# Kernel optimization log

Hardware: AMD Instinct MI355X
Metric: run time of the kernel (lower is better)

## Reference

```python
import jax, jax.numpy as jnp
import numpy as np

L, H, N = 4096, 256, 64  # seq_len, hidden_size, hippo_n
EPS = 1e-5


def setup_inputs() -> dict:
    key = jax.random.key(0)
    ks = jax.random.split(key, 8)
    x = jax.random.normal(ks[0], (L, H), jnp.float32)
    # S4D-Lin style initialization for the diagonal SSM (H independent SSMs of state size N)
    Lambda_re = -0.5 * jnp.ones((H, N), jnp.float32)
    Lambda_im = jnp.tile(jnp.pi * jnp.arange(N, dtype=jnp.float32), (H, 1))
    B_re = jnp.ones((H, N), jnp.float32)
    B_im = jnp.zeros((H, N), jnp.float32)
    C_re = jax.random.normal(ks[1], (H, N), jnp.float32) * (0.5 ** 0.5)
    C_im = jax.random.normal(ks[2], (H, N), jnp.float32) * (0.5 ** 0.5)
    D = jax.random.normal(ks[3], (H,), jnp.float32)
    log_step = jax.random.uniform(ks[4], (H,), jnp.float32,
                                  minval=jnp.log(0.001), maxval=jnp.log(0.1))
    ln_w = jnp.ones((H,), jnp.float32)
    ln_b = jnp.zeros((H,), jnp.float32)
    sc = 1.0 / jnp.sqrt(jnp.float32(H))
    W1 = jax.random.normal(ks[5], (H, H), jnp.float32) * sc
    b1 = jnp.zeros((H,), jnp.float32)
    W2 = jax.random.normal(ks[6], (H, H), jnp.float32) * sc
    b2 = jnp.zeros((H,), jnp.float32)
    return {"x": x, "Lambda_re": Lambda_re, "Lambda_im": Lambda_im,
            "B_re": B_re, "B_im": B_im, "C_re": C_re, "C_im": C_im,
            "D": D, "log_step": log_step, "ln_w": ln_w, "ln_b": ln_b,
            "W1": W1, "b1": b1, "W2": W2, "b2": b2}


def reference(x, Lambda_re, Lambda_im, B_re, B_im, C_re, C_im, D, log_step,
              ln_w, ln_b, W1, b1, W2, b2):
    skip = x
    # per-token LayerNorm over the H feature axis (eqx.nn.LayerNorm, eps=1e-5)
    mu = jnp.mean(x, axis=-1, keepdims=True)
    var = jnp.mean(jnp.square(x - mu), axis=-1, keepdims=True)
    xn = (x - mu) / jnp.sqrt(var + EPS) * ln_w + ln_b  # [L, H]

    # ZOH discretization of the diagonal SSM (the cell.ssm(L) step)
    Lam = Lambda_re + 1j * Lambda_im                     # [H, N] complex64
    dt = jnp.exp(log_step)[:, None]                      # [H, 1]
    Ab = jnp.exp(Lam * dt)                               # [H, N]
    Bb = (Ab - 1.0) / Lam * (B_re + 1j * B_im)           # [H, N]
    C = C_re + 1j * C_im                                 # [H, N]

    def step(s, u):  # s: [H, N] complex state, u: [H] input at one time step
        s = Ab * s + Bb * u[:, None]
        y = 2.0 * jnp.einsum('hn,hn->h', C, s).real + D * u
        return s, y

    s0 = jnp.zeros((H, N), jnp.complex64)
    hidden, ys = jax.lax.scan(step, s0, xn)              # ys: [L, H]

    g = jax.nn.gelu(ys)
    out = (g @ W1.T + b1) * jax.nn.sigmoid(g @ W2.T + b2)  # GLU epilogue
    return (hidden, skip + out)
```

## Files before the change

kernel.cpp:

```cpp
#include <hip/hip_runtime.h>
#include <hip/hip_bf16.h>

#define LSEQ 4096
#define HDIM 256
#define NS   64
#define PC   32
#define MC   128

typedef __attribute__((ext_vector_type(8))) short short8;
typedef __attribute__((ext_vector_type(4))) float floatx4;

__device__ __forceinline__ short b16(float x) {
    __hip_bfloat16 h = __float2bfloat16(x);
    return *(reinterpret_cast<short*>(&h));
}
__device__ __forceinline__ unsigned int pk2(float a, float b) {
    return (unsigned int)(unsigned short)b16(a) | ((unsigned int)(unsigned short)b16(b) << 16);
}
__device__ __forceinline__ void cmul(float& xr, float& xi, float yr, float yi) {
    float r = xr * yr - xi * yi;
    float i = xr * yi + xi * yr;
    xr = r; xi = i;
}

__global__ __launch_bounds__(256) void k_pre(const float* __restrict__ x,
                                             const float* __restrict__ lnw,
                                             const float* __restrict__ lnb,
                                             const float* __restrict__ W1,
                                             const float* __restrict__ W2,
                                             float* __restrict__ xnT,
                                             unsigned short* __restrict__ w1b,
                                             unsigned short* __restrict__ w2b) {
    int t = threadIdx.x;
    if (blockIdx.x >= 256) {
        int g = (blockIdx.x - 256) * 256 + t;
        float4 a = ((const float4*)W1)[g];
        float4 c = ((const float4*)W2)[g];
        ushort4 o1, o2;
        o1.x = (unsigned short)b16(a.x); o1.y = (unsigned short)b16(a.y);
        o1.z = (unsigned short)b16(a.z); o1.w = (unsigned short)b16(a.w);
        o2.x = (unsigned short)b16(c.x); o2.y = (unsigned short)b16(c.y);
        o2.z = (unsigned short)b16(c.z); o2.w = (unsigned short)b16(c.w);
        ((ushort4*)w1b)[g] = o1;
        ((ushort4*)w2b)[g] = o2;
        return;
    }
    __shared__ float tile[16][257];
    __shared__ float smu[16], srs[16];
    int l0 = blockIdx.x * 16;
#pragma unroll
    for (int i = 0; i < 16; ++i)
        tile[i][t] = x[(size_t)(l0 + i) * HDIM + t];
    __syncthreads();
    int wv = t >> 6, lane = t & 63;
#pragma unroll
    for (int k = 0; k < 4; ++k) {
        int i = wv * 4 + k;
        float s = 0.f, s2 = 0.f;
#pragma unroll
        for (int q = 0; q < 4; ++q) {
            float v = tile[i][lane + 64 * q];
            s += v; s2 += v * v;
        }
#pragma unroll
        for (int o = 32; o; o >>= 1) {
            s  += __shfl_xor(s, o);
            s2 += __shfl_xor(s2, o);
        }
        if (lane == 0) {
            float m = s * (1.0f / HDIM);
            smu[i] = m;
            srs[i] = rsqrtf(s2 * (1.0f / HDIM) - m * m + 1e-5f);
        }
    }
    __syncthreads();
    float wh = lnw[t], bh = lnb[t];
    float o[16];
#pragma unroll
    for (int i = 0; i < 16; ++i)
        o[i] = (tile[i][t] - smu[i]) * srs[i] * wh + bh;
    float4* dst = (float4*)(xnT + (size_t)t * LSEQ + l0);
#pragma unroll
    for (int k = 0; k < 4; ++k)
        dst[k] = make_float4(o[4 * k], o[4 * k + 1], o[4 * k + 2], o[4 * k + 3]);
}

__device__ __forceinline__ void ssm_consts(const float* Lre, const float* Lim,
                                           const float* Bre, const float* Bim,
                                           float dt, int idx,
                                           float& are, float& aim, float& bre, float& bim) {
    float lre = Lre[idx], lim = Lim[idx];
    float er = expf(lre * dt);
    float sa, ca;
    sincosf(lim * dt, &sa, &ca);
    are = er * ca; aim = er * sa;
    float inv = 1.0f / (lre * lre + lim * lim);
    float nre = are - 1.0f, nim = aim;
    float tre = (nre * lre + nim * lim) * inv;
    float tim = (nim * lre - nre * lim) * inv;
    float br = Bre[idx], bi = Bim[idx];
    bre = tre * br - tim * bi;
    bim = tre * bi + tim * br;
}

__global__ __launch_bounds__(1024) void k_scan(const float* __restrict__ xnT,
                                               const float* __restrict__ Lre,
                                               const float* __restrict__ Lim,
                                               const float* __restrict__ Bre,
                                               const float* __restrict__ Bim,
                                               const float* __restrict__ Cre,
                                               const float* __restrict__ Cim,
                                               const float* __restrict__ Dv,
                                               const float* __restrict__ lstep,
                                               __hip_bfloat16* __restrict__ gb,
                                               float* __restrict__ hid,
                                               int interleaved) {
    __shared__ __align__(16) unsigned char ldsb[60672];
    short* ubf = (short*)(ldsb);
    short* Xm  = (short*)(ldsb + 8704);
    float* Ff  = (float*)(ldsb + 43520);
    short* S0s = (short*)(ldsb + 43520);
    float* Kt  = (float*)(ldsb + 60160);

    int h = blockIdx.x;
    int tid = threadIdx.x;
    int wv = __builtin_amdgcn_readfirstlane(tid) >> 6;
    int lane = tid & 63;
    int l15 = lane & 15, q = lane >> 4;
    int mt = wv >> 1, nt = wv & 1;
    const float* uh = xnT + (size_t)h * LSEQ;

    float dt = expf(lstep[h]);
    float Dh = Dv[h];

    float are, aim, bre, bim;
    ssm_consts(Lre, Lim, Bre, Bim, dt, h * NS + lane, are, aim, bre, bim);
    float cre = Cre[h * NS + lane], cim = Cim[h * NS + lane];

    float A2r = are, A2i = aim;   cmul(A2r, A2i, are, aim);
    float A4r = A2r, A4i = A2i;   cmul(A4r, A4i, A2r, A2i);
    float A8r = A4r, A8i = A4i;   cmul(A8r, A8i, A4r, A4i);
    float A16r = A8r, A16i = A8i;  cmul(A16r, A16i, A8r, A8i);
    float A32r = A16r, A32i = A16i; cmul(A32r, A32i, A16r, A16i);
    float A64r = A32r, A64i = A32i; cmul(A64r, A64i, A32r, A32i);

    {
        int i4 = tid * 4;
        float4 v = *(const float4*)(uh + i4);
        int c = i4 >> 7, col = i4 & 127;
        unsigned int* d = (unsigned int*)(ubf + c * 136 + col);
        d[0] = pk2(v.x, v.y);
        d[1] = pk2(v.z, v.w);
    }

    {
        float cbre = cre * bre - cim * bim;
        float cbim = cre * bim + cim * bre;
        float pr = 1.f, pi = 0.f;
        if (wv & 1) cmul(pr, pi, A8r, A8i);
        if (wv & 2) cmul(pr, pi, A16r, A16i);
        if (wv & 4) cmul(pr, pi, A32r, A32i);
        if (wv & 8) cmul(pr, pi, A64r, A64i);
#pragma unroll
        for (int i = 0; i < 8; ++i) {
            float kj = 2.f * (cbre * pr - cbim * pi);
#pragma unroll
            for (int o = 1; o <= 32; o <<= 1) kj += __shfl_xor(kj, o);
            if (lane == 0) Kt[8 * wv + i] = kj;
            cmul(pr, pi, are, aim);
        }
    }

    {
        int v = 15 - wv;
        float pr = 1.f, pi = 0.f;
        if (v & 1) cmul(pr, pi, A8r, A8i);
        if (v & 2) cmul(pr, pi, A16r, A16i);
        if (v & 4) cmul(pr, pi, A32r, A32i);
        if (v & 8) cmul(pr, pi, A64r, A64i);
        short8 rr, ri;
#pragma unroll
        for (int i = 0; i < 8; ++i) {
            rr[7 - i] = b16(bre * pr - bim * pi);
            ri[7 - i] = b16(bre * pi + bim * pr);
            cmul(pr, pi, are, aim);
        }
        *(short8*)(Xm + lane * 136 + 8 * wv) = rr;
        *(short8*)(Xm + (64 + lane) * 136 + 8 * wv) = ri;
    }
    __syncthreads();

    {
        floatx4 fa = (floatx4){0.f, 0.f, 0.f, 0.f};
#pragma unroll
        for (int ks = 0; ks < 4; ++ks) {
            short8 am = *(short8*)(Xm + (16 * mt + l15) * 136 + 32 * ks + 8 * q);
            short8 bu = *(short8*)(ubf + (16 * nt + l15) * 136 + 32 * ks + 8 * q);
            fa = __builtin_amdgcn_mfma_f32_16x16x32_bf16(am, bu, fa, 0, 0, 0);
        }
        int c = 16 * nt + l15;
        float* fp = Ff + c * 130;
        int sbase = 16 * mt + 4 * q;
#pragma unroll
        for (int reg = 0; reg < 4; ++reg) {
            int s = sbase + reg;
            fp[(mt < 4) ? s : (1 + s)] = fa[reg];
        }
    }
    __syncthreads();

    if (wv == 0) {
        float a128r = A64r, a128i = A64i;
        cmul(a128r, a128i, A64r, A64i);
        float sre = 0.f, sim = 0.f;
        for (int c = 0; c < PC; ++c) {
            float fre = Ff[c * 130 + lane];
            float fim = Ff[c * 130 + 65 + lane];
            ((unsigned int*)(ldsb + 43520 + 272 * c))[lane] = pk2(sre, sim);
            float nr = fmaf(a128r, sre, fmaf(-a128i, sim, fre));
            float ni = fmaf(a128r, sim, fmaf( a128i, sre, fim));
            sre = nr; sim = ni;
        }
        if (interleaved) {
            ((float2*)hid)[h * NS + lane] = make_float2(sre, sim);
        } else {
            hid[h * NS + lane] = sre;
        }
    } else {
        float A15r = A8r, A15i = A8i;
        cmul(A15r, A15i, A4r, A4i);
        cmul(A15r, A15i, A2r, A2i);
        cmul(A15r, A15i, are, aim);
        float pr = 1.f, pi = 0.f;
        if (wv & 1) cmul(pr, pi, are, aim);
        if (wv & 2) cmul(pr, pi, A2r, A2i);
        if (wv & 4) cmul(pr, pi, A4r, A4i);
        if (wv & 8) cmul(pr, pi, A8r, A8i);
#pragma unroll
        for (int i = 0; i < 9; ++i) {
            int t = (wv - 1) + 15 * i;
            if (t < 128) {
                float er =  2.f * (cre * pr - cim * pi);
                float en = -2.f * (cre * pi + cim * pr);
                ((unsigned int*)(ldsb + 8704 + 272 * t))[lane] = pk2(er, en);
            }
            cmul(pr, pi, A15r, A15i);
        }
    }

    floatx4 Y = (floatx4){0.f, 0.f, 0.f, 0.f};
    {
        int row = 16 * mt + l15;
#pragma unroll
        for (int ks = 0; ks < 4; ++ks) {
            short8 ta;
#pragma unroll
            for (int e = 0; e < 8; ++e) {
                int col = 32 * ks + 8 * q + e;
                float kv = Kt[(row - col) & 127];
                ta[e] = (col <= row) ? b16(kv) : (short)0;
            }
            short8 bu = *(short8*)(ubf + (16 * nt + l15) * 136 + 32 * ks + 8 * q);
            Y = __builtin_amdgcn_mfma_f32_16x16x32_bf16(ta, bu, Y, 0, 0, 0);
        }
    }
    __syncthreads();

#pragma unroll
    for (int ks = 0; ks < 4; ++ks) {
        short8 ea = *(short8*)(Xm + (16 * mt + l15) * 136 + 32 * ks + 8 * q);
        short8 sf = *(short8*)(S0s + (16 * nt + l15) * 136 + 32 * ks + 8 * q);
        Y = __builtin_amdgcn_mfma_f32_16x16x32_bf16(ea, sf, Y, 0, 0, 0);
    }

    {
        int c = 16 * nt + l15;
#pragma unroll
        for (int reg = 0; reg < 4; ++reg) {
            int t = 16 * mt + 4 * q + reg;
            int l = c * MC + t;
            float u = uh[l];
            float y = Y[reg] + Dh * u;
            float z = 0.7978845608028654f * fmaf(0.044715f, y * y * y, y);
            float e = __expf(2.f * z);
            float th = 1.f - 2.f / (e + 1.f);
            float gg = 0.5f * y * (1.f + th);
            gb[((size_t)l << 8) + h] = __float2bfloat16(gg);
        }
    }
}

__global__ __launch_bounds__(64) void k_glu_mfma(const unsigned short* __restrict__ gbs,
                                                 const unsigned short* __restrict__ w1b,
                                                 const unsigned short* __restrict__ w2b,
                                                 const float* __restrict__ b1v,
                                                 const float* __restrict__ b2v,
                                                 const float* __restrict__ x,
                                                 float* __restrict__ out) {
    int bx = blockIdx.x;
    int m0 = (bx >> 4) * 32;
    int n0 = (bx & 15) * 16;
    int lane = threadIdx.x;
    int t = lane & 15, q = lane >> 4;

    floatx4 acc[2][2];
    acc[0][0] = (floatx4){0,0,0,0}; acc[0][1] = (floatx4){0,0,0,0};
    acc[1][0] = (floatx4){0,0,0,0}; acc[1][1] = (floatx4){0,0,0,0};

    const unsigned short* A0 = gbs + (size_t)(m0 + t) * HDIM + q * 8;
    const unsigned short* A1 = A0 + 16 * HDIM;
    const unsigned short* B1 = w1b + (size_t)(n0 + t) * HDIM + q * 8;
    const unsigned short* B2 = w2b + (size_t)(n0 + t) * HDIM + q * 8;

#pragma unroll
    for (int ks = 0; ks < 8; ++ks) {
        int off = ks * 32;
        short8 a0 = *(const short8*)(A0 + off);
        short8 a1 = *(const short8*)(A1 + off);
        short8 b1 = *(const short8*)(B1 + off);
        short8 b2 = *(const short8*)(B2 + off);
        acc[0][0] = __builtin_amdgcn_mfma_f32_16x16x32_bf16(a0, b1, acc[0][0], 0, 0, 0);
        acc[1][0] = __builtin_amdgcn_mfma_f32_16x16x32_bf16(a1, b1, acc[1][0], 0, 0, 0);
        acc[0][1] = __builtin_amdgcn_mfma_f32_16x16x32_bf16(a0, b2, acc[0][1], 0, 0, 0);
        acc[1][1] = __builtin_amdgcn_mfma_f32_16x16x32_bf16(a1, b2, acc[1][1], 0, 0, 0);
    }

    int hh = n0 + t;
    float bb1 = b1v[hh], bb2 = b2v[hh];
#pragma unroll
    for (int mt = 0; mt < 2; ++mt) {
#pragma unroll
        for (int reg = 0; reg < 4; ++reg) {
            int l = m0 + mt * 16 + q * 4 + reg;
            float a  = acc[mt][0][reg] + bb1;
            float sg = 1.f / (1.f + __expf(-(acc[mt][1][reg] + bb2)));
            out[(size_t)l * HDIM + hh] = fmaf(a, sg, x[(size_t)l * HDIM + hh]);
        }
    }
}

extern "C" void kernel_launch(void* const* d_in, const int* in_sizes, int n_in,
                              void* d_out, int out_size, void* d_ws, size_t ws_size,
                              hipStream_t stream) {
    (void)in_sizes; (void)n_in; (void)ws_size;
    const float* x     = (const float*)d_in[0];
    const float* Lre   = (const float*)d_in[1];
    const float* Lim   = (const float*)d_in[2];
    const float* Bre   = (const float*)d_in[3];
    const float* Bim   = (const float*)d_in[4];
    const float* Cre   = (const float*)d_in[5];
    const float* Cim   = (const float*)d_in[6];
    const float* Dv    = (const float*)d_in[7];
    const float* lstep = (const float*)d_in[8];
    const float* lnw   = (const float*)d_in[9];
    const float* lnb   = (const float*)d_in[10];
    const float* W1    = (const float*)d_in[11];
    const float* b1    = (const float*)d_in[12];
    const float* W2    = (const float*)d_in[13];
    const float* b2    = (const float*)d_in[14];

    float* ws   = (float*)d_ws;
    float* xnT  = ws;
    unsigned short* gb  = (unsigned short*)(xnT + (size_t)HDIM * LSEQ);
    unsigned short* w1b = gb + (size_t)LSEQ * HDIM;
    unsigned short* w2b = w1b + HDIM * HDIM;

    int interleaved = (out_size == LSEQ * HDIM + 2 * HDIM * NS) ? 1 : 0;
    float* hid  = (float*)d_out;
    float* outp = (float*)d_out + (interleaved ? 2 * HDIM * NS : HDIM * NS);

    k_pre      <<<256 + 64, 256, 0, stream>>>(x, lnw, lnb, W1, W2, xnT, w1b, w2b);
    k_scan     <<<HDIM, 1024, 0, stream>>>(xnT, Lre, Lim, Bre, Bim, Cre, Cim,
                                           Dv, lstep, (__hip_bfloat16*)gb, hid, interleaved);
    k_glu_mfma <<<128 * 16, 64, 0, stream>>>(gb, w1b, w2b, b1, b2, x, outp);
}
```

Baseline: 115.9 us.

## Split SSM scan block per channel into two 512-thread halves

The chunked-scan kernel now launches two 512-thread blocks per hidden channel instead of one 1024-thread block. Each block redundantly builds the chunk-state tables and runs the serial 32-chunk state recurrence, then computes the output for only half of the chunk columns. The D*u skip term is also read from the bf16 LDS copy instead of reloading fp32 from global memory. The aim is better occupancy and spreading the work over more CUs, at the cost of duplicated setup and recurrence work plus slightly lower precision on the skip term.

```diff
diff --git a/kernel.cpp b/kernel.cpp
--- a/kernel.cpp
+++ b/kernel.cpp
@@ -13,6 +13,10 @@
 __device__ __forceinline__ short b16(float x) {
     __hip_bfloat16 h = __float2bfloat16(x);
     return *(reinterpret_cast<short*>(&h));
+}
+__device__ __forceinline__ float bf2f(unsigned short u) {
+    unsigned int v = ((unsigned int)u) << 16;
+    return __uint_as_float(v);
 }
 __device__ __forceinline__ unsigned int pk2(float a, float b) {
     return (unsigned int)(unsigned short)b16(a) | ((unsigned int)(unsigned short)b16(b) << 16);
@@ -103,18 +107,18 @@
     bim = tre * bi + tim * br;
 }
 
-__global__ __launch_bounds__(1024) void k_scan(const float* __restrict__ xnT,
-                                               const float* __restrict__ Lre,
-                                               const float* __restrict__ Lim,
-                                               const float* __restrict__ Bre,
-                                               const float* __restrict__ Bim,
-                                               const float* __restrict__ Cre,
-                                               const float* __restrict__ Cim,
-                                               const float* __restrict__ Dv,
-                                               const float* __restrict__ lstep,
-                                               __hip_bfloat16* __restrict__ gb,
-                                               float* __restrict__ hid,
-                                               int interleaved) {
+__global__ __launch_bounds__(512) void k_scan(const float* __restrict__ xnT,
+                                              const float* __restrict__ Lre,
+                                              const float* __restrict__ Lim,
+                                              const float* __restrict__ Bre,
+                                              const float* __restrict__ Bim,
+                                              const float* __restrict__ Cre,
+                                              const float* __restrict__ Cim,
+                                              const float* __restrict__ Dv,
+                                              const float* __restrict__ lstep,
+                                              __hip_bfloat16* __restrict__ gb,
+                                              float* __restrict__ hid,
+                                              int interleaved) {
     __shared__ __align__(16) unsigned char ldsb[60672];
     short* ubf = (short*)(ldsb);
     short* Xm  = (short*)(ldsb + 8704);
@@ -122,12 +126,11 @@
     short* S0s = (short*)(ldsb + 43520);
     float* Kt  = (float*)(ldsb + 60160);
 
-    int h = blockIdx.x;
+    int h = blockIdx.x >> 1, half = blockIdx.x & 1;
     int tid = threadIdx.x;
     int wv = __builtin_amdgcn_readfirstlane(tid) >> 6;
     int lane = tid & 63;
     int l15 = lane & 15, q = lane >> 4;
-    int mt = wv >> 1, nt = wv & 1;
     const float* uh = xnT + (size_t)h * LSEQ;
 
     float dt = expf(lstep[h]);
@@ -145,66 +148,82 @@
     float A64r = A32r, A64i = A32i; cmul(A64r, A64i, A32r, A32i);
 
     {
-        int i4 = tid * 4;
-        float4 v = *(const float4*)(uh + i4);
-        int c = i4 >> 7, col = i4 & 127;
+        int i8 = tid * 8;
+        float4 v0 = *(const float4*)(uh + i8);
+        float4 v1 = *(const float4*)(uh + i8 + 4);
+        int c = i8 >> 7, col = i8 & 127;
         unsigned int* d = (unsigned int*)(ubf + c * 136 + col);
-        d[0] = pk2(v.x, v.y);
-        d[1] = pk2(v.z, v.w);
+        d[0] = pk2(v0.x, v0.y);
+        d[1] = pk2(v0.z, v0.w);
+        d[2] = pk2(v1.x, v1.y);
+        d[3] = pk2(v1.z, v1.w);
     }
 
     {
         float cbre = cre * bre - cim * bim;
         float cbim = cre * bim + cim * bre;
         float pr = 1.f, pi = 0.f;
-        if (wv & 1) cmul(pr, pi, A8r, A8i);
-        if (wv & 2) cmul(pr, pi, A16r, A16i);
-        if (wv & 4) cmul(pr, pi, A32r, A32i);
-        if (wv & 8) cmul(pr, pi, A64r, A64i);
-#pragma unroll
-        for (int i = 0; i < 8; ++i) {
+        if (wv & 1) cmul(pr, pi, A16r, A16i);
+        if (wv & 2) cmul(pr, pi, A32r, A32i);
+        if (wv & 4) cmul(pr, pi, A64r, A64i);
+#pragma unroll
+        for (int i = 0; i < 16; ++i) {
             float kj = 2.f * (cbre * pr - cbim * pi);
 #pragma unroll
             for (int o = 1; o <= 32; o <<= 1) kj += __shfl_xor(kj, o);
-            if (lane == 0) Kt[8 * wv + i] = kj;
+            if (lane == 0) Kt[16 * wv + i] = kj;
             cmul(pr, pi, are, aim);
         }
     }
 
     {
-        int v = 15 - wv;
+        int v = 7 - wv;
         float pr = 1.f, pi = 0.f;
-        if (v & 1) cmul(pr, pi, A8r, A8i);
-        if (v & 2) cmul(pr, pi, A16r, A16i);
-        if (v & 4) cmul(pr, pi, A32r, A32i);
-        if (v & 8) cmul(pr, pi, A64r, A64i);
-        short8 rr, ri;
-#pragma unroll
-        for (int i = 0; i < 8; ++i) {
-            rr[7 - i] = b16(bre * pr - bim * pi);
-            ri[7 - i] = b16(bre * pi + bim * pr);
+        if (v & 1) cmul(pr, pi, A16r, A16i);
+        if (v & 2) cmul(pr, pi, A32r, A32i);
+        if (v & 4) cmul(pr, pi, A64r, A64i);
+        short8 rrB, riB, rrA, riA;
+#pragma unroll
+        for (int e = 7; e >= 0; --e) {
+            rrB[e] = b16(bre * pr - bim * pi);
+            riB[e] = b16(bre * pi + bim * pr);
             cmul(pr, pi, are, aim);
         }
-        *(short8*)(Xm + lane * 136 + 8 * wv) = rr;
-        *(short8*)(Xm + (64 + lane) * 136 + 8 * wv) = ri;
-    }
-    __syncthreads();
-
-    {
-        floatx4 fa = (floatx4){0.f, 0.f, 0.f, 0.f};
+#pragma unroll
+        for (int e = 7; e >= 0; --e) {
+            rrA[e] = b16(bre * pr - bim * pi);
+            riA[e] = b16(bre * pi + bim * pr);
+            if (e) cmul(pr, pi, are, aim);
+        }
+        *(short8*)(Xm + lane * 136 + 16 * wv) = rrA;
+        *(short8*)(Xm + lane * 136 + 16 * wv + 8) = rrB;
+        *(short8*)(Xm + (64 + lane) * 136 + 16 * wv) = riA;
+        *(short8*)(Xm + (64 + lane) * 136 + 16 * wv + 8) = riB;
+    }
+    __syncthreads();
+
+    {
+        floatx4 fa[2];
+        fa[0] = (floatx4){0.f, 0.f, 0.f, 0.f};
+        fa[1] = (floatx4){0.f, 0.f, 0.f, 0.f};
 #pragma unroll
         for (int ks = 0; ks < 4; ++ks) {
-            short8 am = *(short8*)(Xm + (16 * mt + l15) * 136 + 32 * ks + 8 * q);
-            short8 bu = *(short8*)(ubf + (16 * nt + l15) * 136 + 32 * ks + 8 * q);
-            fa = __builtin_amdgcn_mfma_f32_16x16x32_bf16(am, bu, fa, 0, 0, 0);
-        }
-        int c = 16 * nt + l15;
-        float* fp = Ff + c * 130;
-        int sbase = 16 * mt + 4 * q;
-#pragma unroll
-        for (int reg = 0; reg < 4; ++reg) {
-            int s = sbase + reg;
-            fp[(mt < 4) ? s : (1 + s)] = fa[reg];
+            short8 am = *(short8*)(Xm + (16 * wv + l15) * 136 + 32 * ks + 8 * q);
+#pragma unroll
+            for (int ct = 0; ct < 2; ++ct) {
+                short8 bu = *(short8*)(ubf + (16 * ct + l15) * 136 + 32 * ks + 8 * q);
+                fa[ct] = __builtin_amdgcn_mfma_f32_16x16x32_bf16(am, bu, fa[ct], 0, 0, 0);
+            }
+        }
+#pragma unroll
+        for (int ct = 0; ct < 2; ++ct) {
+            int c = 16 * ct + l15;
+            float* fp = Ff + c * 130;
+            int s = 16 * wv + 4 * q;
+#pragma unroll
+            for (int reg = 0; reg < 4; ++reg) {
+                fp[(wv < 4) ? (s + reg) : (1 + s + reg)] = fa[ct][reg];
+            }
         }
     }
     __syncthreads();
@@ -221,36 +240,36 @@
             float ni = fmaf(a128r, sim, fmaf( a128i, sre, fim));
             sre = nr; sim = ni;
         }
-        if (interleaved) {
-            ((float2*)hid)[h * NS + lane] = make_float2(sre, sim);
-        } else {
-            hid[h * NS + lane] = sre;
+        if (half == 1) {
+            if (interleaved) {
+                ((float2*)hid)[h * NS + lane] = make_float2(sre, sim);
+            } else {
+                hid[h * NS + lane] = sre;
+            }
         }
     } else {
-        float A15r = A8r, A15i = A8i;
-        cmul(A15r, A15i, A4r, A4i);
-        cmul(A15r, A15i, A2r, A2i);
-        cmul(A15r, A15i, are, aim);
+        float A7r = A4r, A7i = A4i;
+        cmul(A7r, A7i, A2r, A2i);
+        cmul(A7r, A7i, are, aim);
         float pr = 1.f, pi = 0.f;
         if (wv & 1) cmul(pr, pi, are, aim);
         if (wv & 2) cmul(pr, pi, A2r, A2i);
         if (wv & 4) cmul(pr, pi, A4r, A4i);
-        if (wv & 8) cmul(pr, pi, A8r, A8i);
-#pragma unroll
-        for (int i = 0; i < 9; ++i) {
-            int t = (wv - 1) + 15 * i;
+#pragma unroll
+        for (int i = 0; i < 19; ++i) {
+            int t = (wv - 1) + 7 * i;
             if (t < 128) {
                 float er =  2.f * (cre * pr - cim * pi);
                 float en = -2.f * (cre * pi + cim * pr);
                 ((unsigned int*)(ldsb + 8704 + 272 * t))[lane] = pk2(er, en);
             }
-            cmul(pr, pi, A15r, A15i);
+            cmul(pr, pi, A7r, A7i);
         }
     }
 
     floatx4 Y = (floatx4){0.f, 0.f, 0.f, 0.f};
     {
-        int row = 16 * mt + l15;
+        int row = 16 * wv + l15;
 #pragma unroll
         for (int ks = 0; ks < 4; ++ks) {
             short8 ta;
@@ -260,7 +279,7 @@
                 float kv = Kt[(row - col) & 127];
                 ta[e] = (col <= row) ? b16(kv) : (short)0;
             }
-            short8 bu = *(short8*)(ubf + (16 * nt + l15) * 136 + 32 * ks + 8 * q);
+            short8 bu = *(short8*)(ubf + (16 * half + l15) * 136 + 32 * ks + 8 * q);
             Y = __builtin_amdgcn_mfma_f32_16x16x32_bf16(ta, bu, Y, 0, 0, 0);
         }
     }
@@ -268,18 +287,18 @@
 
 #pragma unroll
     for (int ks = 0; ks < 4; ++ks) {
-        short8 ea = *(short8*)(Xm + (16 * mt + l15) * 136 + 32 * ks + 8 * q);
-        short8 sf = *(short8*)(S0s + (16 * nt + l15) * 136 + 32 * ks + 8 * q);
+        short8 ea = *(short8*)(Xm + (16 * wv + l15) * 136 + 32 * ks + 8 * q);
+        short8 sf = *(short8*)(S0s + (16 * half + l15) * 136 + 32 * ks + 8 * q);
         Y = __builtin_amdgcn_mfma_f32_16x16x32_bf16(ea, sf, Y, 0, 0, 0);
     }
 
     {
-        int c = 16 * nt + l15;
+        int c = 16 * half + l15;
 #pragma unroll
         for (int reg = 0; reg < 4; ++reg) {
-            int t = 16 * mt + 4 * q + reg;
+            int t = 16 * wv + 4 * q + reg;
             int l = c * MC + t;
-            float u = uh[l];
+            float u = bf2f((unsigned short)ubf[c * 136 + t]);
             float y = Y[reg] + Dh * u;
             float z = 0.7978845608028654f * fmaf(0.044715f, y * y * y, y);
             float e = __expf(2.f * z);
@@ -370,7 +389,7 @@
     float* outp = (float*)d_out + (interleaved ? 2 * HDIM * NS : HDIM * NS);
 
     k_pre      <<<256 + 64, 256, 0, stream>>>(x, lnw, lnb, W1, W2, xnT, w1b, w2b);
-    k_scan     <<<HDIM, 1024, 0, stream>>>(xnT, Lre, Lim, Bre, Bim, Cre, Cim,
-                                           Dv, lstep, (__hip_bfloat16*)gb, hid, interleaved);
+    k_scan     <<<2 * HDIM, 512, 0, stream>>>(xnT, Lre, Lim, Bre, Bim, Cre, Cim,
+                                              Dv, lstep, (__hip_bfloat16*)gb, hid, interleaved);
     k_glu_mfma <<<128 * 16, 64, 0, stream>>>(gb, w1b, w2b, b1, b2, x, outp);
 }
```

After: 115.6 us. No clear change (-0.3%).
